# Kernel optimization log

Measured on AMD Instinct MI355X. Metric: run time of the kernel, lower is better.

## Reference

```python
import jax, jax.numpy as jnp
import numpy as np

N, D_IN, D = 4096, 1024, 1024


def setup_inputs() -> dict:
    key = jax.random.key(0)
    ks = jax.random.split(key, 9)
    inputs = jax.random.normal(ks[0], (N, D_IN), jnp.float32)
    # Topological parent pointers: children come before parents (parent[i] > i);
    # root is node N-1 whose 'parent' is the dummy sink slot N.
    rng = np.random.default_rng(0)
    parent = np.minimum(np.arange(N) + rng.integers(1, 8, size=N), N - 1)
    parent[N - 1] = N
    parent = jnp.asarray(parent, jnp.int32)

    def lin_w(k, fan_in, fan_out):
        s = 1.0 / np.sqrt(fan_in)
        return jax.random.uniform(k, (fan_in, fan_out), jnp.float32, -s, s)

    def lin_b(k, fan_in, fan_out):
        s = 1.0 / np.sqrt(fan_in)
        return jax.random.uniform(k, (fan_out,), jnp.float32, -s, s)

    return {
        "inputs": inputs,
        "parent": parent,
        "Wioux": lin_w(ks[1], D_IN, 3 * D),
        "bioux": lin_b(ks[2], D_IN, 3 * D),
        "Wiouh": lin_w(ks[3], D, 3 * D),
        "biouh": lin_b(ks[4], D, 3 * D),
        "Wfx": lin_w(ks[5], D_IN, D),
        "bfx": lin_b(ks[6], D_IN, D),
        "Wfh": lin_w(ks[7], D, D),
        "bfh": lin_b(ks[8], D, D),
    }


def reference(inputs, parent, Wioux, bioux, Wiouh, biouh, Wfx, bfx, Wfh, bfh):
    n = inputs.shape[0]
    d = Wfh.shape[0]
    # Batched input projections (same math as per-node Linear, hoisted out of the recursion)
    iou_x = inputs @ Wioux + bioux            # [N, 3D]
    fx = inputs @ Wfx + bfx                   # [N, D]
    fx_pad = jnp.concatenate([fx, jnp.zeros((1, d), fx.dtype)], axis=0)
    fx_parent = fx_pad[parent]                # fx(x_parent) for each node, [N, D]
    zero = jnp.zeros((n + 1, d), inputs.dtype)  # slot n is the dummy root sink

    def step(carry, xs):
        sum_h, sum_fc = carry                 # per-node running child aggregates
        t, iou_xt, fxp_t, p = xs
        iou = iou_xt + sum_h[t] @ Wiouh + biouh          # [3D]
        i, o, u = jnp.split(iou, 3)
        c = jax.nn.sigmoid(i) * jnp.tanh(u) + sum_fc[t]   # i*u + sum_k f_k*c_k
        h = jax.nn.sigmoid(o) * jnp.tanh(c)
        # forget gate of this node as a child of its parent p
        f = jax.nn.sigmoid(h @ Wfh + bfh + fxp_t)
        sum_h = sum_h.at[p].add(h)
        sum_fc = sum_fc.at[p].add(f * c)
        return (sum_h, sum_fc), h

    xs = (jnp.arange(n), iou_x, fx_parent, parent)
    _, h_all = jax.lax.scan(step, (zero, zero), xs)
    return h_all                              # hidden state of every node, [N, D]
```

## Files before the change

### kernel.cpp

```cpp
#include <hip/hip_runtime.h>
#include <stdint.h>

typedef __attribute__((ext_vector_type(4))) float f32x4;
typedef __attribute__((ext_vector_type(8))) short s16x8;
typedef __attribute__((ext_vector_type(4))) unsigned short u16x4;
typedef unsigned short ushort_t;

#define NN 4096
#define NBLK 128

#define OFF_AEXT   0ull
#define OFF_BT     25165824ull
#define OFF_IOU    50331648ull
#define OFF_FX     100675584ull
#define OFF_FXP    117452800ull
#define OFF_SFC    134230016ull
#define OFF_CWS    151011328ull
#define OFF_NODES  167788544ull
#define OFF_START  (OFF_NODES + 16384ull)
#define OFF_NLEV   (OFF_START + 16400ull)
#define OFF_CNT    (OFF_NLEV + 1008ull)

__device__ __forceinline__ ushort_t f2bf(float f) {
    unsigned u = __float_as_uint(f);
    unsigned r = (u + 0x7FFFu + ((u >> 16) & 1u)) >> 16;
    return (ushort_t)r;
}
__device__ __forceinline__ float bf2f(ushort_t b) {
    return __uint_as_float(((unsigned)b) << 16);
}
__device__ __forceinline__ float sigm(float x) { return 1.0f / (1.0f + __expf(-x)); }
__device__ __forceinline__ float tanh_f(float x) {
    float e = __expf(-2.0f * fabsf(x));
    float t = (1.0f - e) / (1.0f + e);
    return copysignf(t, x);
}
__device__ __forceinline__ unsigned long long ld_dev64(const void* p) {
    return __hip_atomic_load((const unsigned long long*)p, __ATOMIC_RELAXED,
                             __HIP_MEMORY_SCOPE_AGENT);
}
__device__ __forceinline__ unsigned ld_devu(const unsigned* p) {
    return __hip_atomic_load(p, __ATOMIC_RELAXED, __HIP_MEMORY_SCOPE_AGENT);
}
__device__ __forceinline__ void st_dev(float* p, float v) {
    __hip_atomic_store(p, v, __ATOMIC_RELAXED, __HIP_MEMORY_SCOPE_AGENT);
}
__device__ __forceinline__ void atomAddWg(float* p, float v) {
    __hip_atomic_fetch_add(p, v, __ATOMIC_RELAXED, __HIP_MEMORY_SCOPE_WORKGROUP);
}
__device__ __forceinline__ void gload16(const void* g, void* l) {
    __builtin_amdgcn_global_load_lds((const __attribute__((address_space(1))) unsigned*)g,
                                     (__attribute__((address_space(3))) unsigned*)l, 16, 0, 0);
}
__device__ __forceinline__ f32x4 shx4(f32x4 v, int m) {
    f32x4 r;
    r[0] = __shfl_xor(v[0], m); r[1] = __shfl_xor(v[1], m);
    r[2] = __shfl_xor(v[2], m); r[3] = __shfl_xor(v[3], m);
    return r;
}

__global__ void k_build_aext(const float* __restrict__ inputs, ushort_t* __restrict__ aext) {
    int t = blockIdx.x;
    int k0 = threadIdx.x * 4;
    f32x4 v = *(const f32x4*)(inputs + (size_t)t * 1024 + k0);
    u16x4 hi, lo;
#pragma unroll
    for (int j = 0; j < 4; ++j) {
        float f = v[j];
        ushort_t hb = f2bf(f);
        float fr = f - bf2f(hb);
        hi[j] = hb; lo[j] = f2bf(fr);
    }
    size_t base = (size_t)t * 3072;
    *(u16x4*)(aext + base + k0)        = hi;
    *(u16x4*)(aext + base + 1024 + k0) = lo;
    *(u16x4*)(aext + base + 2048 + k0) = hi;
}

__global__ void k_build_bt(const float* __restrict__ Wioux, const float* __restrict__ Wfx,
                           ushort_t* __restrict__ bt) {
    __shared__ float ld[64][65];
    int k0 = blockIdx.x * 64, n0 = blockIdx.y * 64;
    const float* src; int scol, sstr;
    if (n0 < 3072) { src = Wioux; scol = n0; sstr = 3072; }
    else           { src = Wfx;   scol = n0 - 3072; sstr = 1024; }
    int tid = threadIdx.x;
    int nl = tid & 63, kh = tid >> 6;
#pragma unroll
    for (int i = 0; i < 16; ++i) {
        int kl = kh * 16 + i;
        ld[kl][nl] = src[(size_t)(k0 + kl) * sstr + scol + nl];
    }
    __syncthreads();
    int nl2 = tid >> 2, kq = tid & 3;
#pragma unroll
    for (int i2 = 0; i2 < 4; ++i2) {
        int kb = kq * 16 + i2 * 4;
        u16x4 hi, lo;
#pragma unroll
        for (int j = 0; j < 4; ++j) {
            float f = ld[kb + j][nl2];
            ushort_t hb = f2bf(f);
            hi[j] = hb; lo[j] = f2bf(f - bf2f(hb));
        }
        size_t ob = (size_t)(n0 + nl2) * 3072 + k0 + kb;
        *(u16x4*)(bt + ob)        = hi;
        *(u16x4*)(bt + ob + 1024) = hi;
        *(u16x4*)(bt + ob + 2048) = lo;
    }
}

__global__ void k_sched(const int* __restrict__ parent, unsigned* __restrict__ g_nodes,
                        unsigned* __restrict__ g_start, unsigned* __restrict__ g_nlev) {
    __shared__ unsigned lvl[4097];
    __shared__ ushort_t par[4096];
    __shared__ unsigned cnts[4100];
    __shared__ unsigned curs[4100];
    int lane = threadIdx.x;
    for (int i = lane; i < 4097; i += 64) lvl[i] = 0;
    for (int i = lane; i < 4100; i += 64) cnts[i] = 0;
    for (int i = lane; i < 4096; i += 64) par[i] = (ushort_t)parent[i];
    __syncthreads();
    for (int base = 0; base < 4096; base += 64) {
        int t = base + lane;
        int p = par[t];
        unsigned prev = lvl[t];
        while (true) {
            atomicMax(&lvl[p], prev + 1);
            __syncthreads();
            unsigned cur = lvl[t];
            int ch = (cur != prev);
            prev = cur;
            if (!__any(ch)) break;
            __syncthreads();
        }
        __syncthreads();
    }
    unsigned maxl = 0;
    for (int t = lane; t < 4096; t += 64) {
        unsigned l = lvl[t];
        maxl = max(maxl, l);
        atomicAdd(&cnts[l], 1u);
    }
#pragma unroll
    for (int o = 32; o; o >>= 1) maxl = max(maxl, (unsigned)__shfl_xor((int)maxl, o));
    __syncthreads();
    unsigned carry = 0;
    for (int base = 0; base < 4100; base += 64) {
        int i = base + lane;
        unsigned v = (i < 4100) ? cnts[i] : 0u;
        unsigned orig = v;
#pragma unroll
        for (int o = 1; o < 64; o <<= 1) {
            unsigned n = __shfl_up(v, o);
            if (lane >= o) v += n;
        }
        unsigned excl = carry + v - orig;
        if (i < 4100) { curs[i] = excl; g_start[i] = excl; }
        carry += (unsigned)__shfl((int)v, 63);
    }
    __syncthreads();
    for (int t = lane; t < 4096; t += 64) {
        unsigned slot = atomicAdd(&curs[lvl[t]], 1u);
        g_nodes[slot] = (unsigned)t;
    }
    if (lane == 0) *g_nlev = maxl + 1;
}

__launch_bounds__(256)
__global__ void k_gemm(const ushort_t* __restrict__ A, const ushort_t* __restrict__ B,
                       const float* __restrict__ bioux, const float* __restrict__ biouh,
                       const float* __restrict__ bfx,
                       float* __restrict__ iou, float* __restrict__ fx) {
    __shared__ ushort_t As[128 * 32];
    __shared__ ushort_t Bs[128 * 32];
    int tid = threadIdx.x;
    int w = tid >> 6, l = tid & 63;
    int m0 = blockIdx.x * 128, n0 = blockIdx.y * 128;
    int wr = w >> 1, wc = w & 1;
    f32x4 acc[4][4];
    f32x4 z = {0.f, 0.f, 0.f, 0.f};
#pragma unroll
    for (int a = 0; a < 4; ++a)
#pragma unroll
        for (int b = 0; b < 4; ++b) acc[a][b] = z;

    for (int k0 = 0; k0 < 3072; k0 += 32) {
        __syncthreads();
#pragma unroll
        for (int i = 0; i < 2; ++i) {
            int qb = i * 256 + w * 64;
            int q = qb + l;
            int row = q >> 2, ksp = q & 3;
            int ksl = ksp ^ (row & 3);
            gload16(A + (size_t)(m0 + row) * 3072 + k0 + ksl * 8, (char*)As + qb * 16);
            gload16(B + (size_t)(n0 + row) * 3072 + k0 + ksl * 8, (char*)Bs + qb * 16);
        }
        __syncthreads();
        s16x8 av[4], bv[4];
#pragma unroll
        for (int fr = 0; fr < 4; ++fr) {
            int ra = wr * 64 + fr * 16 + (l & 15);
            av[fr] = *(const s16x8*)((const char*)As + ra * 64 + ((((l >> 4) ^ (ra & 3)) & 3) << 4));
            int rb = wc * 64 + fr * 16 + (l & 15);
            bv[fr] = *(const s16x8*)((const char*)Bs + rb * 64 + ((((l >> 4) ^ (rb & 3)) & 3) << 4));
        }
#pragma unroll
        for (int fr = 0; fr < 4; ++fr)
#pragma unroll
            for (int fc = 0; fc < 4; ++fc)
                acc[fr][fc] = __builtin_amdgcn_mfma_f32_16x16x32_bf16(av[fr], bv[fc], acc[fr][fc], 0, 0, 0);
    }
#pragma unroll
    for (int fc = 0; fc < 4; ++fc) {
        int col = n0 + wc * 64 + fc * 16 + (l & 15);
        bool isiou = col < 3072;
        float badd = isiou ? (bioux[col] + biouh[col]) : bfx[col - 3072];
#pragma unroll
        for (int fr = 0; fr < 4; ++fr) {
            int r0 = m0 + wr * 64 + fr * 16 + ((l >> 4) << 2);
#pragma unroll
            for (int jj = 0; jj < 4; ++jj) {
                float v2 = acc[fr][fc][jj] + badd;
                if (isiou) iou[(size_t)(r0 + jj) * 3072 + col] = v2;
                else       fx[(size_t)(r0 + jj) * 1024 + (col - 3072)] = v2;
            }
        }
    }
}

__global__ void k_fxp(const int* __restrict__ parent, const float* __restrict__ fx,
                      const float* __restrict__ bfh, float* __restrict__ fxp,
                      float* __restrict__ sfc, unsigned* __restrict__ cnt) {
    int t = blockIdx.x;
    int d = threadIdx.x * 4;
    f32x4 z = {0.f, 0.f, 0.f, 0.f};
    if (t < 4096) {
        int p = parent[t];
        f32x4 add = (p < 4096) ? *(const f32x4*)(fx + ((size_t)p << 10) + d) : z;
        f32x4 bv = *(const f32x4*)(bfh + d);
        *(f32x4*)(fxp + ((size_t)t << 10) + d) = bv + add;
        *(f32x4*)(sfc + ((size_t)t << 10) + d) = z;
    } else {
        *(f32x4*)(sfc + ((size_t)t << 10) + d) = z;
        for (int i = threadIdx.x; i < 4100; i += 256) cnt[i] = 0u;
    }
}

__launch_bounds__(512, 2)
__global__ void k_tree(const float* __restrict__ Wiouh, const float* __restrict__ Wfh,
                       const int* __restrict__ parent,
                       float* iou, float* sfc, float* cws,
                       const float* __restrict__ fxp,
                       const unsigned* __restrict__ g_nodes, const unsigned* __restrict__ g_start,
                       const unsigned* __restrict__ g_nlev,
                       unsigned* cnt, float* outf) {
    __shared__ char hbufc[8 * 4096];
    __shared__ f32x4 part[8][8][8];
    __shared__ ushort_t nd[4096];
    __shared__ ushort_t par[4096];
    __shared__ unsigned st[4100];
    __shared__ int bailflag;

    int tid = threadIdx.x;
    int w = tid >> 6;
    int d0 = blockIdx.x << 3;
    int rb = tid >> 3, cq = tid & 7;

    if (tid == 0) bailflag = 0;
    for (int i = tid; i < 4096; i += 512) nd[i] = (ushort_t)g_nodes[i];
    for (int i = tid; i < 4096; i += 512) par[i] = (ushort_t)parent[i];
    for (int i = tid; i < 4100; i += 512) st[i] = g_start[i];

    f32x4 wv[16];
    {
        const float* wb; size_t strd; int coff;
        if (cq < 6) { wb = Wiouh; strd = 3072; coff = (cq >> 1) * 1024 + d0 + (cq & 1) * 4; }
        else        { wb = Wfh;   strd = 1024; coff = d0 + (cq - 6) * 4; }
#pragma unroll
        for (int m16 = 0; m16 < 16; ++m16)
            wv[m16] = *(const f32x4*)(wb + (size_t)(rb * 16 + m16) * strd + coff);
    }
    unsigned nlev = *g_nlev;
    if (nlev > 4096u) nlev = 4096u;
    __syncthreads();

    bool bailed = false;
    for (unsigned L = 0; L < nlev; ++L) {
        unsigned s0 = st[L], s1 = st[L + 1];
        if (s0 > 4096u) s0 = 4096u;
        if (s1 > 4096u) s1 = 4096u;
        if (s1 < s0) s1 = s0;
        int m = (int)(s1 - s0);

        for (int idx = tid; idx < (m << 3); idx += 512) {
            int s = idx >> 3, j = idx & 7;
            int t = nd[s0 + s];
            int d = d0 + j;
            size_t b3 = (size_t)t * 3072 + d;
            float vi = iou[b3];
            float vo = iou[b3 + 1024];
            float vu = iou[b3 + 2048];
            float sf = sfc[((size_t)t << 10) + d];
            float cc = sigm(vi) * tanh_f(vu) + sf;
            float hh = sigm(vo) * tanh_f(cc);
            cws[((size_t)t << 10) + d] = cc;
            st_dev(outf + ((size_t)t << 10) + d, hh);
        }
        __syncthreads();

        if (tid == 0) {
            __hip_atomic_fetch_add(cnt + L, 1u, __ATOMIC_RELEASE, __HIP_MEMORY_SCOPE_AGENT);
            if (!bailed) {
                int sp = 0;
                while (ld_devu(cnt + L) < (unsigned)NBLK) {
                    __builtin_amdgcn_s_sleep(2);
                    if (++sp > (1 << 14)) { bailflag = 1; break; }
                }
            }
        }
        __syncthreads();
        bailed = bailed || (bailflag != 0);

        for (int ch = 0; ch < m; ch += 8) {
            int cm = min(8, m - ch);
            int items = cm << 9;
            for (int q = tid; q < items; q += 512) {
                int s = q >> 9, r = q & 511;
                int t = nd[s0 + ch + s];
                unsigned long long v = ld_dev64(outf + ((size_t)t << 10) + (r << 1));
                *(unsigned long long*)(hbufc + (s << 12) + ((r << 3) ^ (((r >> 3) & 3) << 4))) = v;
            }
            __syncthreads();
            f32x4 acc[8];
            f32x4 z = {0.f, 0.f, 0.f, 0.f};
#pragma unroll
            for (int s = 0; s < 8; ++s) acc[s] = z;
#pragma unroll
            for (int s = 0; s < 8; ++s) {
                if (s < cm) {
#pragma unroll
                    for (int ip = 0; ip < 4; ++ip) {
                        f32x4 h4 = *(const f32x4*)(hbufc + (s << 12) + (rb << 6) +
                                                   (((ip ^ (rb & 3))) << 4));
#pragma unroll
                        for (int t4 = 0; t4 < 4; ++t4)
                            acc[s] += h4[t4] * wv[ip * 4 + t4];
                    }
                }
            }
#pragma unroll
            for (int s = 0; s < 8; ++s) {
                if (s < cm) {
                    f32x4 v = acc[s];
                    v += shx4(v, 8);
                    v += shx4(v, 16);
                    v += shx4(v, 32);
                    if ((tid & 56) == 0) part[s][w][cq] = v;
                }
            }
            __syncthreads();
            if (tid < (cm << 5)) {
                int s = tid >> 5, c = tid & 31;
                int cq2 = c >> 2, j = c & 3;
                float sum = 0.f;
#pragma unroll
                for (int w8 = 0; w8 < 8; ++w8) sum += part[s][w8][cq2][j];
                int t = nd[s0 + ch + s];
                int p = par[t];
                if (c < 24) {
                    atomAddWg(iou + (size_t)p * 3072 + (c >> 3) * 1024 + d0 + (c & 7), sum);
                } else {
                    int d = d0 + (c & 7);
                    float fv = sigm(sum + fxp[((size_t)t << 10) + d]);
                    float cv = cws[((size_t)t << 10) + d];
                    atomAddWg(sfc + (((size_t)p) << 10) + d, fv * cv);
                }
            }
            __syncthreads();
        }
    }
}

extern "C" void kernel_launch(void* const* d_in, const int* in_sizes, int n_in,
                              void* d_out, int out_size, void* d_ws, size_t ws_size,
                              hipStream_t stream) {
    const float* inputs = (const float*)d_in[0];
    const int* parent   = (const int*)d_in[1];
    const float* Wioux  = (const float*)d_in[2];
    const float* bioux  = (const float*)d_in[3];
    const float* Wiouh  = (const float*)d_in[4];
    const float* biouh  = (const float*)d_in[5];
    const float* Wfx    = (const float*)d_in[6];
    const float* bfx    = (const float*)d_in[7];
    const float* Wfh    = (const float*)d_in[8];
    const float* bfh    = (const float*)d_in[9];
    float* outf = (float*)d_out;
    char* ws = (char*)d_ws;

    ushort_t* aext   = (ushort_t*)(ws + OFF_AEXT);
    ushort_t* bt     = (ushort_t*)(ws + OFF_BT);
    float* iou       = (float*)(ws + OFF_IOU);
    float* fx        = (float*)(ws + OFF_FX);
    float* fxp       = (float*)(ws + OFF_FXP);
    float* sfc       = (float*)(ws + OFF_SFC);
    float* cws       = (float*)(ws + OFF_CWS);
    unsigned* g_nodes = (unsigned*)(ws + OFF_NODES);
    unsigned* g_start = (unsigned*)(ws + OFF_START);
    unsigned* g_nlev  = (unsigned*)(ws + OFF_NLEV);
    unsigned* cnt     = (unsigned*)(ws + OFF_CNT);

    k_build_aext<<<dim3(4096), dim3(256), 0, stream>>>(inputs, aext);
    k_build_bt<<<dim3(16, 64), dim3(256), 0, stream>>>(Wioux, Wfx, bt);
    k_sched<<<dim3(1), dim3(64), 0, stream>>>(parent, g_nodes, g_start, g_nlev);
    k_gemm<<<dim3(32, 32), dim3(256), 0, stream>>>(aext, bt, bioux, biouh, bfx, iou, fx);
    k_fxp<<<dim3(4097), dim3(256), 0, stream>>>(parent, fx, bfh, fxp, sfc, cnt);
    k_tree<<<dim3(NBLK), dim3(512), 0, stream>>>(Wiouh, Wfh, parent, iou, sfc, cws, fxp,
                                                 g_nodes, g_start, g_nlev, cnt, outf);
}
```

Before: 12.76 ms.

## Use ALAP level schedule, LDS ring accumulators, and per-block flag barriers in tree kernel

Measured after the change: 10.58 ms. 1.21x faster.

```diff
diff --git a/kernel.cpp b/kernel.cpp
--- a/kernel.cpp
+++ b/kernel.cpp
@@ -7,9 +7,11 @@
 typedef unsigned short ushort_t;
 
 #define NN 4096
-#define NBLK 128
+#define NBLK 256
+#define RING 1024
 
 #define OFF_AEXT   0ull
+#define OFF_FLAGS  0ull
 #define OFF_BT     25165824ull
 #define OFF_IOU    50331648ull
 #define OFF_FX     100675584ull
@@ -18,8 +20,8 @@
 #define OFF_CWS    151011328ull
 #define OFF_NODES  167788544ull
 #define OFF_START  (OFF_NODES + 16384ull)
-#define OFF_NLEV   (OFF_START + 16400ull)
-#define OFF_CNT    (OFF_NLEV + 1008ull)
+#define OFF_MISC   (OFF_START + 16400ull)
+#define OFF_PAR16  (OFF_MISC + 16ull)
 
 __device__ __forceinline__ ushort_t f2bf(float f) {
     unsigned u = __float_as_uint(f);
@@ -38,9 +40,6 @@
 __device__ __forceinline__ unsigned long long ld_dev64(const void* p) {
     return __hip_atomic_load((const unsigned long long*)p, __ATOMIC_RELAXED,
                              __HIP_MEMORY_SCOPE_AGENT);
-}
-__device__ __forceinline__ unsigned ld_devu(const unsigned* p) {
-    return __hip_atomic_load(p, __ATOMIC_RELAXED, __HIP_MEMORY_SCOPE_AGENT);
 }
 __device__ __forceinline__ void st_dev(float* p, float v) {
     __hip_atomic_store(p, v, __ATOMIC_RELAXED, __HIP_MEMORY_SCOPE_AGENT);
@@ -111,39 +110,52 @@
 }
 
 __global__ void k_sched(const int* __restrict__ parent, unsigned* __restrict__ g_nodes,
-                        unsigned* __restrict__ g_start, unsigned* __restrict__ g_nlev) {
-    __shared__ unsigned lvl[4097];
-    __shared__ ushort_t par[4096];
-    __shared__ unsigned cnts[4100];
-    __shared__ unsigned curs[4100];
+                        unsigned* __restrict__ g_start, unsigned* __restrict__ g_misc,
+                        ushort_t* __restrict__ par16_g) {
+    volatile __shared__ unsigned short d16[4096];
+    __shared__ unsigned short par16[4096];
+    __shared__ unsigned short lv16[4096];
+    __shared__ unsigned cnts[4100], curs[4100], mni[4100], mxi[4100];
+    __shared__ unsigned sh_maxd;
     int lane = threadIdx.x;
-    for (int i = lane; i < 4097; i += 64) lvl[i] = 0;
-    for (int i = lane; i < 4100; i += 64) cnts[i] = 0;
-    for (int i = lane; i < 4096; i += 64) par[i] = (ushort_t)parent[i];
-    __syncthreads();
-    for (int base = 0; base < 4096; base += 64) {
+    for (int i = lane; i < 4096; i += 64) {
+        d16[i] = 0xFFFFu;
+        int p = parent[i];
+        par16[i] = (ushort_t)p;
+        par16_g[i] = (ushort_t)p;
+    }
+    for (int i = lane; i < 4100; i += 64) { cnts[i] = 0; mni[i] = 0xFFFFFFFFu; mxi[i] = 0; }
+    __syncthreads();
+    if (lane == 0) d16[4095] = 0;
+    __syncthreads();
+    for (int base = 4032; base >= 0; base -= 64) {
         int t = base + lane;
-        int p = par[t];
-        unsigned prev = lvl[t];
-        while (true) {
-            atomicMax(&lvl[p], prev + 1);
-            __syncthreads();
-            unsigned cur = lvl[t];
-            int ch = (cur != prev);
-            prev = cur;
+        int iter = 0;
+        while (iter++ < 80) {
+            bool ch = false;
+            if (t != 4095 && d16[t] == 0xFFFFu) {
+                int p = par16[t];
+                unsigned short dp = d16[p];
+                if (dp != 0xFFFFu) { d16[t] = (unsigned short)(dp + 1); ch = true; }
+            }
             if (!__any(ch)) break;
-            __syncthreads();
         }
         __syncthreads();
     }
-    unsigned maxl = 0;
-    for (int t = lane; t < 4096; t += 64) {
-        unsigned l = lvl[t];
-        maxl = max(maxl, l);
-        atomicAdd(&cnts[l], 1u);
-    }
-#pragma unroll
-    for (int o = 32; o; o >>= 1) maxl = max(maxl, (unsigned)__shfl_xor((int)maxl, o));
+    unsigned mx = 0;
+    for (int i = lane; i < 4096; i += 64) mx = max(mx, (unsigned)d16[i]);
+#pragma unroll
+    for (int o = 32; o; o >>= 1) mx = max(mx, (unsigned)__shfl_xor((int)mx, o));
+    if (lane == 0) sh_maxd = mx;
+    __syncthreads();
+    unsigned maxd = sh_maxd;
+    for (int i = lane; i < 4096; i += 64) {
+        unsigned s = maxd - (unsigned)d16[i];
+        lv16[i] = (ushort_t)s;
+        atomicAdd(&cnts[s], 1u);
+        atomicMin(&mni[s], (unsigned)i);
+        atomicMax(&mxi[s], (unsigned)i);
+    }
     __syncthreads();
     unsigned carry = 0;
     for (int base = 0; base < 4100; base += 64) {
@@ -160,11 +172,20 @@
         carry += (unsigned)__shfl((int)v, 63);
     }
     __syncthreads();
-    for (int t = lane; t < 4096; t += 64) {
-        unsigned slot = atomicAdd(&curs[lvl[t]], 1u);
-        g_nodes[slot] = (unsigned)t;
-    }
-    if (lane == 0) *g_nlev = maxl + 1;
+    for (int i = lane; i < 4096; i += 64) {
+        unsigned s = lv16[i];
+        unsigned slot = atomicAdd(&curs[s], 1u);
+        g_nodes[slot] = (unsigned)i;
+    }
+    unsigned wm = 0;
+    for (unsigned L = lane; L <= maxd; L += 64) {
+        unsigned lo = mni[L], hi = mxi[L];
+        if (L + 1 <= maxd) { lo = min(lo, mni[L + 1]); hi = max(hi, mxi[L + 1]); }
+        wm = max(wm, hi - lo);
+    }
+#pragma unroll
+    for (int o = 32; o; o >>= 1) wm = max(wm, (unsigned)__shfl_xor((int)wm, o));
+    if (lane == 0) { g_misc[0] = maxd + 1; g_misc[1] = (wm <= (unsigned)(RING - 1)) ? 1u : 0u; }
 }
 
 __launch_bounds__(256)
@@ -231,7 +252,7 @@
 
 __global__ void k_fxp(const int* __restrict__ parent, const float* __restrict__ fx,
                       const float* __restrict__ bfh, float* __restrict__ fxp,
-                      float* __restrict__ sfc, unsigned* __restrict__ cnt) {
+                      float* __restrict__ sfc) {
     int t = blockIdx.x;
     int d = threadIdx.x * 4;
     f32x4 z = {0.f, 0.f, 0.f, 0.f};
@@ -243,49 +264,55 @@
         *(f32x4*)(sfc + ((size_t)t << 10) + d) = z;
     } else {
         *(f32x4*)(sfc + ((size_t)t << 10) + d) = z;
-        for (int i = threadIdx.x; i < 4100; i += 256) cnt[i] = 0u;
-    }
-}
-
-__launch_bounds__(512, 2)
+    }
+}
+
+__global__ void k_zero(uint4* __restrict__ p, int n4) {
+    int i = blockIdx.x * blockDim.x + threadIdx.x;
+    uint4 z = {0u, 0u, 0u, 0u};
+    for (; i < n4; i += gridDim.x * blockDim.x) p[i] = z;
+}
+
+__launch_bounds__(512, 1)
 __global__ void k_tree(const float* __restrict__ Wiouh, const float* __restrict__ Wfh,
-                       const int* __restrict__ parent,
                        float* iou, float* sfc, float* cws,
                        const float* __restrict__ fxp,
                        const unsigned* __restrict__ g_nodes, const unsigned* __restrict__ g_start,
-                       const unsigned* __restrict__ g_nlev,
-                       unsigned* cnt, float* outf) {
-    __shared__ char hbufc[8 * 4096];
-    __shared__ f32x4 part[8][8][8];
+                       const unsigned* __restrict__ g_misc,
+                       unsigned* flags, float* outf, const ushort_t* __restrict__ par16) {
+    __shared__ __align__(16) float ring[RING][20];
+    __shared__ __align__(16) float hbuf[8][1024];
+    __shared__ f32x4 part[8][8][4];
     __shared__ ushort_t nd[4096];
     __shared__ ushort_t par[4096];
     __shared__ unsigned st[4100];
-    __shared__ int bailflag;
 
     int tid = threadIdx.x;
-    int w = tid >> 6;
-    int d0 = blockIdx.x << 3;
-    int rb = tid >> 3, cq = tid & 7;
-
-    if (tid == 0) bailflag = 0;
+    int bid = blockIdx.x;
+    int lane = tid & 63, w = tid >> 6;
+    int d0 = bid << 2;
+    int rc = tid >> 2, cq = tid & 3;
+
     for (int i = tid; i < 4096; i += 512) nd[i] = (ushort_t)g_nodes[i];
-    for (int i = tid; i < 4096; i += 512) par[i] = (ushort_t)parent[i];
+    for (int i = tid; i < 4096; i += 512) par[i] = par16[i];
     for (int i = tid; i < 4100; i += 512) st[i] = g_start[i];
-
-    f32x4 wv[16];
+    for (int i = tid; i < RING * 20; i += 512) ((float*)ring)[i] = 0.f;
+
+    unsigned nlev = g_misc[0];
+    bool ringok = (g_misc[1] != 0u);
+    if (nlev > 4096u) nlev = 4096u;
+
+    f32x4 wv[8];
     {
         const float* wb; size_t strd; int coff;
-        if (cq < 6) { wb = Wiouh; strd = 3072; coff = (cq >> 1) * 1024 + d0 + (cq & 1) * 4; }
-        else        { wb = Wfh;   strd = 1024; coff = d0 + (cq - 6) * 4; }
-#pragma unroll
-        for (int m16 = 0; m16 < 16; ++m16)
-            wv[m16] = *(const f32x4*)(wb + (size_t)(rb * 16 + m16) * strd + coff);
-    }
-    unsigned nlev = *g_nlev;
-    if (nlev > 4096u) nlev = 4096u;
-    __syncthreads();
-
-    bool bailed = false;
+        if (cq < 3) { wb = Wiouh; strd = 3072; coff = cq * 1024 + d0; }
+        else        { wb = Wfh;   strd = 1024; coff = d0; }
+#pragma unroll
+        for (int r8 = 0; r8 < 8; ++r8)
+            wv[r8] = *(const f32x4*)(wb + (size_t)(rc * 8 + r8) * strd + coff);
+    }
+    __syncthreads();
+
     for (unsigned L = 0; L < nlev; ++L) {
         unsigned s0 = st[L], s1 = st[L + 1];
         if (s0 > 4096u) s0 = 4096u;
@@ -293,34 +320,49 @@
         if (s1 < s0) s1 = s0;
         int m = (int)(s1 - s0);
 
-        for (int idx = tid; idx < (m << 3); idx += 512) {
-            int s = idx >> 3, j = idx & 7;
+        for (int idx = tid; idx < (m << 2); idx += 512) {
+            int s = idx >> 2, j = idx & 3;
             int t = nd[s0 + s];
             int d = d0 + j;
+            int slot = t & (RING - 1);
             size_t b3 = (size_t)t * 3072 + d;
-            float vi = iou[b3];
-            float vo = iou[b3 + 1024];
-            float vu = iou[b3 + 2048];
-            float sf = sfc[((size_t)t << 10) + d];
-            float cc = sigm(vi) * tanh_f(vu) + sf;
+            float ri, ro, ru, rf;
+            if (ringok) {
+                ri = ring[slot][j];     ro = ring[slot][4 + j];
+                ru = ring[slot][8 + j]; rf = ring[slot][12 + j];
+                ring[slot][j] = 0.f; ring[slot][4 + j] = 0.f;
+                ring[slot][8 + j] = 0.f; ring[slot][12 + j] = 0.f;
+            } else {
+                ri = ro = ru = 0.f;
+                rf = sfc[((size_t)t << 10) + d];
+            }
+            float vi = iou[b3] + ri;
+            float vo = iou[b3 + 1024] + ro;
+            float vu = iou[b3 + 2048] + ru;
+            float cc = sigm(vi) * tanh_f(vu) + rf;
             float hh = sigm(vo) * tanh_f(cc);
-            cws[((size_t)t << 10) + d] = cc;
+            if (ringok) ring[slot][16 + j] = cc;
+            else        cws[((size_t)t << 10) + d] = cc;
             st_dev(outf + ((size_t)t << 10) + d, hh);
         }
+        asm volatile("s_waitcnt vmcnt(0)" ::: "memory");
         __syncthreads();
-
-        if (tid == 0) {
-            __hip_atomic_fetch_add(cnt + L, 1u, __ATOMIC_RELEASE, __HIP_MEMORY_SCOPE_AGENT);
-            if (!bailed) {
-                int sp = 0;
-                while (ld_devu(cnt + L) < (unsigned)NBLK) {
-                    __builtin_amdgcn_s_sleep(2);
-                    if (++sp > (1 << 14)) { bailflag = 1; break; }
-                }
+        if (tid == 0)
+            __hip_atomic_store(flags + (size_t)L * 256 + bid, 1u,
+                               __ATOMIC_RELAXED, __HIP_MEMORY_SCOPE_AGENT);
+        if (tid < 128) {
+            const unsigned long long* fp =
+                (const unsigned long long*)(flags + (size_t)L * 256) + tid;
+            int sp = 0;
+            while (true) {
+                unsigned long long v = __hip_atomic_load(fp, __ATOMIC_RELAXED,
+                                                         __HIP_MEMORY_SCOPE_AGENT);
+                if ((unsigned)v != 0u && (unsigned)(v >> 32) != 0u) break;
+                __builtin_amdgcn_s_sleep(1);
+                if (++sp > (1 << 17)) break;
             }
         }
         __syncthreads();
-        bailed = bailed || (bailflag != 0);
 
         for (int ch = 0; ch < m; ch += 8) {
             int cm = min(8, m - ch);
@@ -329,7 +371,8 @@
                 int s = q >> 9, r = q & 511;
                 int t = nd[s0 + ch + s];
                 unsigned long long v = ld_dev64(outf + ((size_t)t << 10) + (r << 1));
-                *(unsigned long long*)(hbufc + (s << 12) + ((r << 3) ^ (((r >> 3) & 3) << 4))) = v;
+                *(unsigned long long*)((char*)&hbuf[s][0] +
+                    (((unsigned)(r << 3)) ^ ((((unsigned)r >> 4) & 1u) << 4))) = v;
             }
             __syncthreads();
             f32x4 acc[8];
@@ -340,12 +383,12 @@
             for (int s = 0; s < 8; ++s) {
                 if (s < cm) {
 #pragma unroll
-                    for (int ip = 0; ip < 4; ++ip) {
-                        f32x4 h4 = *(const f32x4*)(hbufc + (s << 12) + (rb << 6) +
-                                                   (((ip ^ (rb & 3))) << 4));
-#pragma unroll
-                        for (int t4 = 0; t4 < 4; ++t4)
-                            acc[s] += h4[t4] * wv[ip * 4 + t4];
+                    for (int ip = 0; ip < 2; ++ip) {
+                        f32x4 h4 = *(const f32x4*)((char*)&hbuf[s][0] +
+                                     (rc << 5) + (((ip ^ ((rc >> 2) & 1)) & 1) << 4));
+#pragma unroll
+                        for (int j4 = 0; j4 < 4; ++j4)
+                            acc[s] += h4[j4] * wv[ip * 4 + j4];
                     }
                 }
             }
@@ -353,28 +396,46 @@
             for (int s = 0; s < 8; ++s) {
                 if (s < cm) {
                     f32x4 v = acc[s];
+                    v += shx4(v, 4);
                     v += shx4(v, 8);
                     v += shx4(v, 16);
                     v += shx4(v, 32);
-                    if ((tid & 56) == 0) part[s][w][cq] = v;
+                    if ((lane & 60) == 0) part[s][w][cq] = v;
                 }
             }
             __syncthreads();
-            if (tid < (cm << 5)) {
-                int s = tid >> 5, c = tid & 31;
-                int cq2 = c >> 2, j = c & 3;
+            int nsc = cm << 4;
+            bool lastch = (ch + 8 >= m);
+            if (tid < nsc) {
+                int s = tid >> 4, c = tid & 15, cq2 = c >> 2, j = c & 3;
                 float sum = 0.f;
 #pragma unroll
                 for (int w8 = 0; w8 < 8; ++w8) sum += part[s][w8][cq2][j];
                 int t = nd[s0 + ch + s];
                 int p = par[t];
-                if (c < 24) {
-                    atomAddWg(iou + (size_t)p * 3072 + (c >> 3) * 1024 + d0 + (c & 7), sum);
+                if (c < 12) {
+                    if (ringok) { if (p < 4096) atomicAdd(&ring[p & (RING - 1)][c], sum); }
+                    else atomAddWg(iou + (size_t)p * 3072 + cq2 * 1024 + d0 + j, sum);
                 } else {
-                    int d = d0 + (c & 7);
+                    int d = d0 + j;
                     float fv = sigm(sum + fxp[((size_t)t << 10) + d]);
-                    float cv = cws[((size_t)t << 10) + d];
-                    atomAddWg(sfc + (((size_t)p) << 10) + d, fv * cv);
+                    float cv = ringok ? ring[t & (RING - 1)][16 + j]
+                                      : cws[((size_t)t << 10) + d];
+                    float pr = fv * cv;
+                    if (ringok) { if (p < 4096) atomicAdd(&ring[p & (RING - 1)][12 + j], pr); }
+                    else atomAddWg(sfc + ((size_t)p << 10) + d, pr);
+                }
+            } else if (ringok && lastch && L + 1 < nlev) {
+                int idx = tid - nsc;
+                unsigned s0n = st[L + 1];
+                int m2 = (int)(st[L + 2] - s0n);
+                int s2 = idx >> 2, g = idx & 3;
+                if (s2 < m2) {
+                    int t2 = nd[s0n + s2];
+                    float v;
+                    if (g < 3) v = iou[(size_t)t2 * 3072 + g * 1024 + d0];
+                    else       v = fxp[((size_t)t2 << 10) + d0];
+                    asm volatile("" :: "v"(v));
                 }
             }
             __syncthreads();
@@ -398,23 +459,25 @@
     float* outf = (float*)d_out;
     char* ws = (char*)d_ws;
 
-    ushort_t* aext   = (ushort_t*)(ws + OFF_AEXT);
-    ushort_t* bt     = (ushort_t*)(ws + OFF_BT);
-    float* iou       = (float*)(ws + OFF_IOU);
-    float* fx        = (float*)(ws + OFF_FX);
-    float* fxp       = (float*)(ws + OFF_FXP);
-    float* sfc       = (float*)(ws + OFF_SFC);
-    float* cws       = (float*)(ws + OFF_CWS);
+    ushort_t* aext    = (ushort_t*)(ws + OFF_AEXT);
+    unsigned* flags   = (unsigned*)(ws + OFF_FLAGS);
+    ushort_t* bt      = (ushort_t*)(ws + OFF_BT);
+    float* iou        = (float*)(ws + OFF_IOU);
+    float* fx         = (float*)(ws + OFF_FX);
+    float* fxp        = (float*)(ws + OFF_FXP);
+    float* sfc        = (float*)(ws + OFF_SFC);
+    float* cws        = (float*)(ws + OFF_CWS);
     unsigned* g_nodes = (unsigned*)(ws + OFF_NODES);
     unsigned* g_start = (unsigned*)(ws + OFF_START);
-    unsigned* g_nlev  = (unsigned*)(ws + OFF_NLEV);
-    unsigned* cnt     = (unsigned*)(ws + OFF_CNT);
+    unsigned* g_misc  = (unsigned*)(ws + OFF_MISC);
+    ushort_t* par16   = (ushort_t*)(ws + OFF_PAR16);
 
     k_build_aext<<<dim3(4096), dim3(256), 0, stream>>>(inputs, aext);
     k_build_bt<<<dim3(16, 64), dim3(256), 0, stream>>>(Wioux, Wfx, bt);
-    k_sched<<<dim3(1), dim3(64), 0, stream>>>(parent, g_nodes, g_start, g_nlev);
+    k_sched<<<dim3(1), dim3(64), 0, stream>>>(parent, g_nodes, g_start, g_misc, par16);
     k_gemm<<<dim3(32, 32), dim3(256), 0, stream>>>(aext, bt, bioux, biouh, bfx, iou, fx);
-    k_fxp<<<dim3(4097), dim3(256), 0, stream>>>(parent, fx, bfh, fxp, sfc, cnt);
-    k_tree<<<dim3(NBLK), dim3(512), 0, stream>>>(Wiouh, Wfh, parent, iou, sfc, cws, fxp,
-                                                 g_nodes, g_start, g_nlev, cnt, outf);
-}
+    k_fxp<<<dim3(4097), dim3(256), 0, stream>>>(parent, fx, bfh, fxp, sfc);
+    k_zero<<<dim3(512), dim3(256), 0, stream>>>((uint4*)flags, (4100 * 256) / 4);
+    k_tree<<<dim3(NBLK), dim3(512), 0, stream>>>(Wiouh, Wfh, iou, sfc, cws, fxp,
+                                                 g_nodes, g_start, g_misc, flags, outf, par16);
+}
```
